# Performance work log

Measured on AMD Instinct MI355X. Metric: run time of the kernel, lower is better.

The kernel has to match this reference:

```python
import jax, jax.numpy as jnp
import numpy as np

B, S, D = 4, 4096, 1024
H, DH = 16, 64            # heads, head dim (D = H*DH)
W = 256                   # local window size; S % W == 0
HID = 2 * D               # GEGLU hidden dim
LN_EPS = 1e-5


def setup_inputs() -> dict:
    key = jax.random.key(0)
    ks = jax.random.split(key, 8)
    w = lambda k, shp: (jax.random.normal(k, shp, jnp.float32) * 0.02)
    return {
        "x": jax.random.normal(ks[0], (B, S, D), jnp.float32),
        "ln1_g": jnp.ones((D,), jnp.float32), "ln1_b": jnp.zeros((D,), jnp.float32),
        "ln2_g": jnp.ones((D,), jnp.float32), "ln2_b": jnp.zeros((D,), jnp.float32),
        "Wq": w(ks[1], (D, D)), "Wk": w(ks[2], (D, D)), "Wv": w(ks[3], (D, D)),
        "Wo": w(ks[4], (D, D)), "bo": jnp.zeros((D,), jnp.float32),
        "W1": w(ks[5], (D, 2 * HID)), "b1": jnp.zeros((2 * HID,), jnp.float32),
        "W2": w(ks[6], (HID, D)), "b2": jnp.zeros((D,), jnp.float32),
    }


def layer_norm(x, g, b):
    mu = jnp.mean(x, axis=-1, keepdims=True)
    var = jnp.mean(jnp.square(x - mu), axis=-1, keepdims=True)
    return (x - mu) * jax.lax.rsqrt(var + LN_EPS) * g + b


def local_causal_attention(x, Wq, Wk, Wv, Wo, bo):
    b, s, d = x.shape
    nw = s // W
    def split_heads(t):  # [b,s,d] -> [b,H,nw,W,DH]
        return t.reshape(b, s, H, DH).transpose(0, 2, 1, 3).reshape(b, H, nw, W, DH)
    q = split_heads(x @ Wq)
    k = split_heads(x @ Wk)
    v = split_heads(x @ Wv)
    # look_backward=1: each window attends to [prev window, current window]
    def with_prev(t):  # [b,H,nw,W,DH] -> [b,H,nw,2W,DH]
        prev = jnp.pad(t, ((0, 0), (0, 0), (1, 0), (0, 0), (0, 0)))[:, :, :-1]
        return jnp.concatenate([prev, t], axis=3)
    kc, vc = with_prev(k), with_prev(v)
    scores = jnp.einsum("bhnqd,bhnkd->bhnqk", q, kc) * (DH ** -0.5)
    # positions: qpos = n*W + i ; kpos = (n-1)*W + j, j in [0,2W)
    n = jnp.arange(nw)[:, None, None]
    i = jnp.arange(W)[None, :, None]
    j = jnp.arange(2 * W)[None, None, :]
    qpos = n * W + i
    kpos = (n - 1) * W + j
    mask = (kpos <= qpos) & (kpos >= 0)  # causal + left-edge padding
    scores = jnp.where(mask[None, None], scores, jnp.finfo(scores.dtype).min)
    attn = jax.nn.softmax(scores, axis=-1)
    out = jnp.einsum("bhnqk,bhnkd->bhnqd", attn, vc)
    out = out.reshape(b, H, s, DH).transpose(0, 2, 1, 3).reshape(b, s, d)
    return out @ Wo + bo


def geglu(x, W1, b1, W2, b2):
    h = x @ W1 + b1
    a, g = jnp.split(h, 2, axis=-1)
    return (a * jax.nn.gelu(g, approximate=False)) @ W2 + b2


def reference(x, ln1_g, ln1_b, ln2_g, ln2_b, Wq, Wk, Wv, Wo, bo, W1, b1, W2, b2):
    x = x + local_causal_attention(layer_norm(x, ln1_g, ln1_b), Wq, Wk, Wv, Wo, bo)
    x = x + geglu(layer_norm(x, ln2_g, ln2_b), W1, b1, W2, b2)
    return x
```

## Files before the change

kernel.cpp:

```cpp
#include <hip/hip_runtime.h>
#include <hip/hip_bf16.h>

typedef __attribute__((ext_vector_type(4))) float f32x4;
typedef __attribute__((ext_vector_type(8))) short bf16x8;
typedef __attribute__((ext_vector_type(8))) unsigned short u16x8;

static __device__ __forceinline__ ushort f2b(float f) {
  union { float f; unsigned u; } v; v.f = f;
  unsigned r = v.u + 0x7fffu + ((v.u >> 16) & 1u);
  return (ushort)(r >> 16);
}

static __device__ __forceinline__ float gelu_fast(float g) {
  const float c0 = 0.7978845608028654f, c1 = 0.044715f;
  const float u = c0 * (g + c1 * g * g * g);
  const float e = __expf(2.0f * u);
  const float t = 1.0f - 2.0f / (e + 1.0f);
  return 0.5f * g * (1.0f + t);
}

static __device__ __forceinline__ void gload_lds16(const void* g, void* l) {
  __builtin_amdgcn_global_load_lds(
      (__attribute__((address_space(1))) void*)(g),
      (__attribute__((address_space(3))) void*)(l), 16, 0, 0);
}

__global__ __launch_bounds__(256) void transpose_cast_kernel(
    const float* __restrict__ W, ushort* __restrict__ Wt, int K, int N) {
  __shared__ float tile[32][33];
  const int n0 = blockIdx.x * 32, k0 = blockIdx.y * 32;
  const int tx = threadIdx.x, ty = threadIdx.y;
#pragma unroll
  for (int r = 0; r < 32; r += 8)
    tile[ty + r][tx] = W[(size_t)(k0 + ty + r) * N + n0 + tx];
  __syncthreads();
#pragma unroll
  for (int r = 0; r < 32; r += 8)
    Wt[(size_t)(n0 + ty + r) * K + k0 + tx] = f2b(tile[tx][ty + r]);
}

__global__ __launch_bounds__(256) void ln_kernel(
    const float* __restrict__ x, const float* __restrict__ g,
    const float* __restrict__ bb, ushort* __restrict__ out) {
  const int row = blockIdx.x;
  const float* xr = x + (size_t)row * 1024;
  const float4 v = *(const float4*)&xr[threadIdx.x * 4];
  float s = v.x + v.y + v.z + v.w;
  float s2 = v.x * v.x + v.y * v.y + v.z * v.z + v.w * v.w;
#pragma unroll
  for (int off = 32; off > 0; off >>= 1) {
    s += __shfl_down(s, off);
    s2 += __shfl_down(s2, off);
  }
  __shared__ float red[8];
  const int lane = threadIdx.x & 63, wv = threadIdx.x >> 6;
  if (lane == 0) { red[wv] = s; red[4 + wv] = s2; }
  __syncthreads();
  s = red[0] + red[1] + red[2] + red[3];
  s2 = red[4] + red[5] + red[6] + red[7];
  const float mu = s * (1.0f / 1024.0f);
  const float rs = rsqrtf(s2 * (1.0f / 1024.0f) - mu * mu + 1e-5f);
  const int c = threadIdx.x * 4;
  ushort4 o;
  o.x = f2b((v.x - mu) * rs * g[c + 0] + bb[c + 0]);
  o.y = f2b((v.y - mu) * rs * g[c + 1] + bb[c + 1]);
  o.z = f2b((v.z - mu) * rs * g[c + 2] + bb[c + 2]);
  o.w = f2b((v.w - mu) * rs * g[c + 3] + bb[c + 3]);
  *(ushort4*)&out[(size_t)row * 1024 + c] = o;
}

template <int MODE>
__global__ __launch_bounds__(512) void gemm256_kernel(
    const ushort* __restrict__ A, const ushort* __restrict__ Bt,
    const int M, const int N, const int K,
    ushort* __restrict__ Cb, float* __restrict__ Cf,
    const float* __restrict__ bias, const float* __restrict__ res) {
  __shared__ __align__(16) ushort lds[3 * 16384];

  const int ntn = N >> 8;
  const int bn = blockIdx.x % ntn;
  const int bm = blockIdx.x / ntn;
  const int tid = threadIdx.x;
  const int l = tid & 63, w = tid >> 6;
  const int wm = w >> 2, wn = w & 3;
  const int fr = l & 15, fq = l >> 4;

  const ushort* Ab = A + (size_t)bm * 256 * K;
  const ushort* Bb = Bt + (size_t)bn * 256 * K;

  const int srow = (l >> 2);
  const int scol = (((l & 3) ^ ((l >> 3) & 3)) * 8);

  f32x4 acc[8][4];
#pragma unroll
  for (int m = 0; m < 8; m++)
#pragma unroll
    for (int n = 0; n < 4; n++) acc[m][n] = (f32x4)0.0f;

  const int NT = K >> 5;

#define STAGE256(t)                                                            \
  {                                                                            \
    const int b3 = (t) % 3;                                                    \
    const size_t kk = (size_t)(t) * 32;                                        \
    _Pragma("unroll") for (int i = 0; i < 2; i++) {                            \
      const int r = (w * 2 + i) * 16 + srow;                                   \
      gload_lds16(Ab + (size_t)r * K + kk + scol,                              \
                  &lds[b3 * 16384 + (w * 2 + i) * 512]);                       \
      gload_lds16(Bb + (size_t)r * K + kk + scol,                              \
                  &lds[b3 * 16384 + 8192 + (w * 2 + i) * 512]);                \
    }                                                                          \
  }

  STAGE256(0);
  STAGE256(1);

  for (int t = 0; t < NT; ++t) {
    if (t + 2 < NT) {
      STAGE256(t + 2);
      asm volatile("s_waitcnt vmcnt(8)" ::: "memory");
    } else if (t + 1 < NT) {
      asm volatile("s_waitcnt vmcnt(4)" ::: "memory");
    } else {
      asm volatile("s_waitcnt vmcnt(0)" ::: "memory");
    }
    __builtin_amdgcn_s_barrier();
    asm volatile("" ::: "memory");

    const ushort* La = &lds[(t % 3) * 16384];
    const ushort* Lb = La + 8192;

    bf16x8 af[8], bf[4];
#pragma unroll
    for (int m = 0; m < 8; m++) {
      const int r = wm * 128 + m * 16 + fr;
      af[m] = *(const bf16x8*)&La[r * 32 + ((fq ^ ((r >> 1) & 3)) * 8)];
    }
#pragma unroll
    for (int n = 0; n < 4; n++) {
      const int r = wn * 64 + n * 16 + fr;
      bf[n] = *(const bf16x8*)&Lb[r * 32 + ((fq ^ ((r >> 1) & 3)) * 8)];
    }

    __builtin_amdgcn_s_setprio(1);
#pragma unroll
    for (int m = 0; m < 8; m++)
#pragma unroll
      for (int n = 0; n < 4; n++)
        acc[m][n] = __builtin_amdgcn_mfma_f32_16x16x32_bf16(af[m], bf[n], acc[m][n], 0, 0, 0);
    __builtin_amdgcn_s_setprio(0);

    asm volatile("" ::: "memory");
    __builtin_amdgcn_s_barrier();
  }
#undef STAGE256

  const int rowb = bm * 256 + wm * 128 + fq * 4;
  const int colb = bn * 256 + wn * 64 + fr;
#pragma unroll
  for (int m = 0; m < 8; m++) {
#pragma unroll
    for (int n = 0; n < 4; n++) {
      const int col = colb + n * 16;
#pragma unroll
      for (int j = 0; j < 4; j++) {
        const int row = rowb + m * 16 + j;
        float vv = acc[m][n][j];
        if (MODE == 0) {
          Cb[(size_t)row * N + col] = f2b(vv);
        } else if (MODE == 2) {
          if (col < 1024) vv *= 0.125f;
          Cb[(size_t)row * N + col] = f2b(vv);
        } else {
          Cf[(size_t)row * N + col] = vv + bias[col] + res[(size_t)row * N + col];
        }
      }
    }
  }
}

__global__ __launch_bounds__(512) void gemm_geglu_kernel(
    const ushort* __restrict__ A, const ushort* __restrict__ W1t,
    const float* __restrict__ b1, ushort* __restrict__ U) {
  const int K = 1024;
  __shared__ __align__(16) ushort lds[3 * 16384];

  const int bn = blockIdx.x & 15;
  const int bm = blockIdx.x >> 4;
  const int tid = threadIdx.x;
  const int l = tid & 63, w = tid >> 6;
  const int wm = w >> 2, wn = w & 3;
  const int fr = l & 15, fq = l >> 4;

  const ushort* Ab = A + (size_t)bm * 256 * K;
  const ushort* Bab = W1t + (size_t)bn * 128 * K;
  const ushort* Bgb = W1t + (size_t)(2048 + bn * 128) * K;

  const int srow = (l >> 2);
  const int scol = (((l & 3) ^ ((l >> 3) & 3)) * 8);
  const int brow = (tid >> 2);
  const int bscol = (((tid & 3) ^ ((tid >> 3) & 3)) * 8);

  f32x4 acca[8][2], accg[8][2];
#pragma unroll
  for (int m = 0; m < 8; m++)
#pragma unroll
    for (int n = 0; n < 2; n++) { acca[m][n] = (f32x4)0.0f; accg[m][n] = (f32x4)0.0f; }

  const int NT = K >> 5;

#define STAGEGL(t)                                                             \
  {                                                                            \
    const int b3 = (t) % 3;                                                    \
    const size_t kk = (size_t)(t) * 32;                                        \
    _Pragma("unroll") for (int i = 0; i < 2; i++) {                            \
      const int r = (w * 2 + i) * 16 + srow;                                   \
      gload_lds16(Ab + (size_t)r * K + kk + scol,                              \
                  &lds[b3 * 16384 + (w * 2 + i) * 512]);                       \
    }                                                                          \
    gload_lds16(Bab + (size_t)brow * K + kk + bscol,                           \
                &lds[b3 * 16384 + 8192 + w * 512]);                            \
    gload_lds16(Bgb + (size_t)brow * K + kk + bscol,                           \
                &lds[b3 * 16384 + 12288 + w * 512]);                           \
  }

  STAGEGL(0);
  STAGEGL(1);

  for (int t = 0; t < NT; ++t) {
    if (t + 2 < NT) {
      STAGEGL(t + 2);
      asm volatile("s_waitcnt vmcnt(8)" ::: "memory");
    } else if (t + 1 < NT) {
      asm volatile("s_waitcnt vmcnt(4)" ::: "memory");
    } else {
      asm volatile("s_waitcnt vmcnt(0)" ::: "memory");
    }
    __builtin_amdgcn_s_barrier();
    asm volatile("" ::: "memory");

    const ushort* La = &lds[(t % 3) * 16384];
    const ushort* Lba = La + 8192;
    const ushort* Lbg = La + 12288;

    bf16x8 af[8], ba[2], bg[2];
#pragma unroll
    for (int m = 0; m < 8; m++) {
      const int r = wm * 128 + m * 16 + fr;
      af[m] = *(const bf16x8*)&La[r * 32 + ((fq ^ ((r >> 1) & 3)) * 8)];
    }
#pragma unroll
    for (int n = 0; n < 2; n++) {
      const int r = wn * 32 + n * 16 + fr;
      ba[n] = *(const bf16x8*)&Lba[r * 32 + ((fq ^ ((r >> 1) & 3)) * 8)];
      bg[n] = *(const bf16x8*)&Lbg[r * 32 + ((fq ^ ((r >> 1) & 3)) * 8)];
    }

    __builtin_amdgcn_s_setprio(1);
#pragma unroll
    for (int m = 0; m < 8; m++)
#pragma unroll
      for (int n = 0; n < 2; n++) {
        acca[m][n] = __builtin_amdgcn_mfma_f32_16x16x32_bf16(af[m], ba[n], acca[m][n], 0, 0, 0);
        accg[m][n] = __builtin_amdgcn_mfma_f32_16x16x32_bf16(af[m], bg[n], accg[m][n], 0, 0, 0);
      }
    __builtin_amdgcn_s_setprio(0);

    asm volatile("" ::: "memory");
    __builtin_amdgcn_s_barrier();
  }
#undef STAGEGL

  const int rowb = bm * 256 + wm * 128 + fq * 4;
  const int colb = bn * 128 + wn * 32 + fr;
#pragma unroll
  for (int m = 0; m < 8; m++) {
#pragma unroll
    for (int n = 0; n < 2; n++) {
      const int col = colb + n * 16;
      const float b1a = b1[col];
      const float b1g = b1[2048 + col];
#pragma unroll
      for (int j = 0; j < 4; j++) {
        const int row = rowb + m * 16 + j;
        const float a = acca[m][n][j] + b1a;
        const float gg = accg[m][n][j] + b1g;
        U[(size_t)row * 2048 + col] = f2b(a * gelu_fast(gg));
      }
    }
  }
}

__global__ __launch_bounds__(256, 3) void attn_kernel(
    const ushort* __restrict__ Q, const ushort* __restrict__ Kb,
    const ushort* __restrict__ Vb, ushort* __restrict__ O, const int qs) {
  const int bx = blockIdx.x;
  const int n = bx & 15;
  const int h = (bx >> 4) & 15;
  const int b = bx >> 8;
  const int tid = threadIdx.x;
  const int lane = tid & 63, wv = tid >> 6;
  const int fr = lane & 15, fq = lane >> 4;

  __shared__ __align__(16) ushort Kl[64 * 72];
  __shared__ __align__(16) ushort Vt[64 * 70];
  __shared__ __align__(16) ushort Pl[4][64 * 68];

  const size_t qrow0 = (size_t)b * 4096 + (size_t)n * 256;

  bf16x8 qf[4][2];
#pragma unroll
  for (int m = 0; m < 4; m++)
#pragma unroll
    for (int kh = 0; kh < 2; kh++)
      qf[m][kh] = *(const bf16x8*)&Q[(qrow0 + wv * 64 + m * 16 + fr) * qs + h * 64 + kh * 32 + fq * 8];

  f32x4 oacc[4][4];
#pragma unroll
  for (int m = 0; m < 4; m++)
#pragma unroll
    for (int d = 0; d < 4; d++) oacc[m][d] = (f32x4)0.0f;

  float lsum[4][4];
#pragma unroll
  for (int m = 0; m < 4; m++)
#pragma unroll
    for (int j = 0; j < 4; j++) lsum[m][j] = 0.0f;

  const int c0 = (n == 0) ? 4 : 0;
  for (int c = c0; c < 8; c++) {
    const size_t kvrow0 =
        (size_t)((long long)b * 4096 + (long long)n * 256 + (long long)c * 64 - 256);
#pragma unroll
    for (int p = 0; p < 2; p++) {
      const int s = tid + p * 256;
      const int rr = s >> 3, cs2 = s & 7;
      *(u16x8*)&Kl[rr * 72 + cs2 * 8] =
          *(const u16x8*)&Kb[(kvrow0 + rr) * qs + h * 64 + cs2 * 8];
      const u16x8 vvv = *(const u16x8*)&Vb[(kvrow0 + rr) * qs + h * 64 + cs2 * 8];
#pragma unroll
      for (int i = 0; i < 8; i++) Vt[(cs2 * 8 + i) * 70 + rr] = vvv[i];
    }
    __syncthreads();

    if (c <= wv + 4) {
      const bool diag = (c == wv + 4);
#pragma unroll
      for (int nn = 0; nn < 4; nn++) {
        f32x4 sa[4];
#pragma unroll
        for (int m = 0; m < 4; m++) sa[m] = (f32x4)0.0f;
#pragma unroll
        for (int kh = 0; kh < 2; kh++) {
          const bf16x8 bk = *(const bf16x8*)&Kl[(nn * 16 + fr) * 72 + kh * 32 + fq * 8];
#pragma unroll
          for (int m = 0; m < 4; m++)
            sa[m] = __builtin_amdgcn_mfma_f32_16x16x32_bf16(qf[m][kh], bk, sa[m], 0, 0, 0);
        }
#pragma unroll
        for (int m = 0; m < 4; m++)
#pragma unroll
          for (int j = 0; j < 4; j++) {
            float p = __expf(sa[m][j]);
            if (diag && (nn * 16 + fr > m * 16 + fq * 4 + j)) p = 0.0f;
            lsum[m][j] += p;
            Pl[wv][(m * 16 + fq * 4 + j) * 68 + nn * 16 + fr] = f2b(p);
          }
      }
      __builtin_amdgcn_s_setprio(1);
#pragma unroll
      for (int kh = 0; kh < 2; kh++) {
        bf16x8 pa[4];
#pragma unroll
        for (int m = 0; m < 4; m++)
          pa[m] = *(const bf16x8*)&Pl[wv][(m * 16 + fr) * 68 + kh * 32 + fq * 8];
#pragma unroll
        for (int d = 0; d < 4; d++) {
          const bf16x8 vb = *(const bf16x8*)&Vt[(d * 16 + fr) * 70 + kh * 32 + fq * 8];
#pragma unroll
          for (int m = 0; m < 4; m++)
            oacc[m][d] = __builtin_amdgcn_mfma_f32_16x16x32_bf16(pa[m], vb, oacc[m][d], 0, 0, 0);
        }
      }
      __builtin_amdgcn_s_setprio(0);
    }
    __syncthreads();
  }

  float rl[4][4];
#pragma unroll
  for (int m = 0; m < 4; m++)
#pragma unroll
    for (int j = 0; j < 4; j++) {
      float t = lsum[m][j];
      t += __shfl_xor(t, 1);
      t += __shfl_xor(t, 2);
      t += __shfl_xor(t, 4);
      t += __shfl_xor(t, 8);
      rl[m][j] = 1.0f / t;
    }

#pragma unroll
  for (int m = 0; m < 4; m++)
#pragma unroll
    for (int d = 0; d < 4; d++)
#pragma unroll
      for (int j = 0; j < 4; j++) {
        const float o = oacc[m][d][j] * rl[m][j];
        O[(qrow0 + wv * 64 + m * 16 + fq * 4 + j) * 1024 + h * 64 + d * 16 + fr] = f2b(o);
      }
}

extern "C" void kernel_launch(void* const* d_in, const int* in_sizes, int n_in,
                              void* d_out, int out_size, void* d_ws, size_t ws_size,
                              hipStream_t stream) {
  (void)in_sizes; (void)n_in; (void)out_size; (void)ws_size;
  const float* x     = (const float*)d_in[0];
  const float* ln1_g = (const float*)d_in[1];
  const float* ln1_b = (const float*)d_in[2];
  const float* ln2_g = (const float*)d_in[3];
  const float* ln2_b = (const float*)d_in[4];
  const float* Wq    = (const float*)d_in[5];
  const float* Wk    = (const float*)d_in[6];
  const float* Wv    = (const float*)d_in[7];
  const float* Wo    = (const float*)d_in[8];
  const float* bo    = (const float*)d_in[9];
  const float* W1    = (const float*)d_in[10];
  const float* b1    = (const float*)d_in[11];
  const float* W2    = (const float*)d_in[12];
  const float* b2    = (const float*)d_in[13];

  char* ws = (char*)d_ws;
  const size_t MB = 1ull << 20;
  ushort* WQKVT = (ushort*)(ws + 0 * MB);
  ushort* WOT = (ushort*)(ws + 6 * MB);
  ushort* W1T = (ushort*)(ws + 8 * MB);
  ushort* W2T = (ushort*)(ws + 16 * MB);
  ushort* LN1 = (ushort*)(ws + 20 * MB);
  ushort* ATT = LN1;
  ushort* QKV = (ushort*)(ws + 52 * MB);
  ushort* LN2 = (ushort*)(ws + 52 * MB);
  ushort* U   = (ushort*)(ws + 84 * MB);
  float*  X1  = (float*)d_out;
  float*  OUT = (float*)d_out;

  const dim3 tb(32, 8);
  transpose_cast_kernel<<<dim3(32, 32), tb, 0, stream>>>(Wq, WQKVT, 1024, 1024);
  transpose_cast_kernel<<<dim3(32, 32), tb, 0, stream>>>(Wk, WQKVT + (size_t)1024 * 1024, 1024, 1024);
  transpose_cast_kernel<<<dim3(32, 32), tb, 0, stream>>>(Wv, WQKVT + (size_t)2048 * 1024, 1024, 1024);
  transpose_cast_kernel<<<dim3(32, 32), tb, 0, stream>>>(Wo, WOT, 1024, 1024);
  transpose_cast_kernel<<<dim3(128, 32), tb, 0, stream>>>(W1, W1T, 1024, 4096);
  transpose_cast_kernel<<<dim3(32, 64), tb, 0, stream>>>(W2, W2T, 2048, 1024);

  ln_kernel<<<16384, 256, 0, stream>>>(x, ln1_g, ln1_b, LN1);

  gemm256_kernel<2><<<64 * 12, 512, 0, stream>>>(LN1, WQKVT, 16384, 3072, 1024,
                                                 QKV, nullptr, nullptr, nullptr);

  attn_kernel<<<1024, 256, 0, stream>>>(QKV, QKV + 1024, QKV + 2048, ATT, 3072);

  gemm256_kernel<1><<<64 * 4, 512, 0, stream>>>(ATT, WOT, 16384, 1024, 1024,
                                                nullptr, X1, bo, x);

  ln_kernel<<<16384, 256, 0, stream>>>(X1, ln2_g, ln2_b, LN2);

  gemm_geglu_kernel<<<64 * 16, 512, 0, stream>>>(LN2, W1T, b1, U);

  gemm256_kernel<1><<<64 * 4, 512, 0, stream>>>(U, W2T, 16384, 1024, 2048,
                                                nullptr, OUT, b2, X1);
}
```

Measured before the change: 557.0 us.

## Restructure GEMM main loops into 4-stage split-phase pipeline with XCD swizzle

Result: no change. 550.9 us (-1.1%).

```diff
diff --git a/kernel.cpp b/kernel.cpp
--- a/kernel.cpp
+++ b/kernel.cpp
@@ -23,6 +23,13 @@
   __builtin_amdgcn_global_load_lds(
       (__attribute__((address_space(1))) void*)(g),
       (__attribute__((address_space(3))) void*)(l), 16, 0, 0);
+}
+
+#define MFMA_BF16 __builtin_amdgcn_mfma_f32_16x16x32_bf16
+
+static __device__ __forceinline__ int xcd_swz(int bid, int nwg) {
+  const int q = nwg >> 3;
+  return (bid & 7) * q + (bid >> 3);
 }
 
 __global__ __launch_bounds__(256) void transpose_cast_kernel(
@@ -70,26 +77,40 @@
 }
 
 template <int MODE>
-__global__ __launch_bounds__(512) void gemm256_kernel(
+__global__ __launch_bounds__(512, 2) void gemm256_kernel(
     const ushort* __restrict__ A, const ushort* __restrict__ Bt,
     const int M, const int N, const int K,
     ushort* __restrict__ Cb, float* __restrict__ Cf,
     const float* __restrict__ bias, const float* __restrict__ res) {
-  __shared__ __align__(16) ushort lds[3 * 16384];
-
+  __shared__ __align__(16) ushort lds[65536];
+
+  const int nwg = gridDim.x;
+  const int bid = xcd_swz((int)blockIdx.x, nwg);
   const int ntn = N >> 8;
-  const int bn = blockIdx.x % ntn;
-  const int bm = blockIdx.x / ntn;
+  const int bn = bid % ntn;
+  const int bm = bid / ntn;
   const int tid = threadIdx.x;
   const int l = tid & 63, w = tid >> 6;
   const int wm = w >> 2, wn = w & 3;
   const int fr = l & 15, fq = l >> 4;
 
-  const ushort* Ab = A + (size_t)bm * 256 * K;
-  const ushort* Bb = Bt + (size_t)bn * 256 * K;
-
-  const int srow = (l >> 2);
-  const int scol = (((l & 3) ^ ((l >> 3) & 3)) * 8);
+  const char* ldsc = (const char*)lds;
+  char* ldscw = (char*)lds;
+
+  const unsigned sl16 = (unsigned)((fq ^ ((fr >> 2) & 3)) * 16);
+  const unsigned aOff = (unsigned)(wm * 8192 + fr * 64) + sl16;
+  const unsigned bOff = 16384u + (unsigned)(wn * 4096 + fr * 64) + sl16;
+  const unsigned aB0 = 0 * 32768u + aOff, aB1 = 1 * 32768u + aOff;
+  const unsigned aB2 = 2 * 32768u + aOff, aB3 = 3 * 32768u + aOff;
+  const unsigned bB0 = 0 * 32768u + bOff, bB1 = 1 * 32768u + bOff;
+  const unsigned bB2 = 2 * 32768u + bOff, bB3 = 3 * 32768u + bOff;
+
+  const int srow = tid >> 2;
+  const int scol = (((tid & 3) ^ ((tid >> 4) & 3)) * 8);
+  const ushort* qA0 = A + (size_t)bm * 256 * K + (size_t)srow * K + scol;
+  const ushort* qA1 = qA0 + (size_t)128 * K;
+  const ushort* qB0 = Bt + (size_t)bn * 256 * K + (size_t)srow * K + scol;
+  const ushort* qB1 = qB0 + (size_t)128 * K;
 
   f32x4 acc[8][4];
 #pragma unroll
@@ -98,62 +119,74 @@
     for (int n = 0; n < 4; n++) acc[m][n] = (f32x4)0.0f;
 
   const int NT = K >> 5;
-
-#define STAGE256(t)                                                            \
+  const unsigned wlds = (unsigned)(w * 1024);
+
+#define GB(aBv, bBv, WSB, DOSTG, VMM, KOFF)                                    \
   {                                                                            \
-    const int b3 = (t) % 3;                                                    \
-    const size_t kk = (size_t)(t) * 32;                                        \
-    _Pragma("unroll") for (int i = 0; i < 2; i++) {                            \
-      const int r = (w * 2 + i) * 16 + srow;                                   \
-      gload_lds16(Ab + (size_t)r * K + kk + scol,                              \
-                  &lds[b3 * 16384 + (w * 2 + i) * 512]);                       \
-      gload_lds16(Bb + (size_t)r * K + kk + scol,                              \
-                  &lds[b3 * 16384 + 8192 + (w * 2 + i) * 512]);                \
-    }                                                                          \
-  }
-
-  STAGE256(0);
-  STAGE256(1);
-
-  for (int t = 0; t < NT; ++t) {
-    if (t + 2 < NT) {
-      STAGE256(t + 2);
-      asm volatile("s_waitcnt vmcnt(8)" ::: "memory");
-    } else if (t + 1 < NT) {
-      asm volatile("s_waitcnt vmcnt(4)" ::: "memory");
-    } else {
-      asm volatile("s_waitcnt vmcnt(0)" ::: "memory");
-    }
-    __builtin_amdgcn_s_barrier();
-    asm volatile("" ::: "memory");
-
-    const ushort* La = &lds[(t % 3) * 16384];
-    const ushort* Lb = La + 8192;
-
-    bf16x8 af[8], bf[4];
-#pragma unroll
-    for (int m = 0; m < 8; m++) {
-      const int r = wm * 128 + m * 16 + fr;
-      af[m] = *(const bf16x8*)&La[r * 32 + ((fq ^ ((r >> 1) & 3)) * 8)];
-    }
-#pragma unroll
-    for (int n = 0; n < 4; n++) {
-      const int r = wn * 64 + n * 16 + fr;
-      bf[n] = *(const bf16x8*)&Lb[r * 32 + ((fq ^ ((r >> 1) & 3)) * 8)];
-    }
-
-    __builtin_amdgcn_s_setprio(1);
-#pragma unroll
-    for (int m = 0; m < 8; m++)
-#pragma unroll
-      for (int n = 0; n < 4; n++)
-        acc[m][n] = __builtin_amdgcn_mfma_f32_16x16x32_bf16(af[m], bf[n], acc[m][n], 0, 0, 0);
-    __builtin_amdgcn_s_setprio(0);
-
-    asm volatile("" ::: "memory");
-    __builtin_amdgcn_s_barrier();
-  }
-#undef STAGE256
+    bf16x8 af[8], bfv[4];                                                      \
+    if (DOSTG) {                                                               \
+      gload_lds16(qA0 + (KOFF), ldscw + (WSB) + wlds);                         \
+      gload_lds16(qA1 + (KOFF), ldscw + (WSB) + 8192 + wlds);                  \
+    }                                                                          \
+    _Pragma("unroll") for (int m = 0; m < 8; m++)                              \
+      af[m] = *(const bf16x8*)(ldsc + (aBv) + m * 1024);                       \
+    bfv[0] = *(const bf16x8*)(ldsc + (bBv));                                   \
+    bfv[1] = *(const bf16x8*)(ldsc + (bBv) + 1024);                            \
+    __builtin_amdgcn_s_barrier();                                              \
+    asm volatile("" ::: "memory");                                             \
+    __builtin_amdgcn_s_setprio(1);                                             \
+    _Pragma("unroll") for (int m = 0; m < 8; m++) {                            \
+      acc[m][0] = MFMA_BF16(af[m], bfv[0], acc[m][0], 0, 0, 0);                \
+      acc[m][1] = MFMA_BF16(af[m], bfv[1], acc[m][1], 0, 0, 0);                \
+    }                                                                          \
+    __builtin_amdgcn_s_setprio(0);                                             \
+    asm volatile("" ::: "memory");                                             \
+    __builtin_amdgcn_s_barrier();                                              \
+    if (DOSTG) {                                                               \
+      gload_lds16(qB0 + (KOFF), ldscw + (WSB) + 16384 + wlds);                 \
+      gload_lds16(qB1 + (KOFF), ldscw + (WSB) + 24576 + wlds);                 \
+    }                                                                          \
+    bfv[2] = *(const bf16x8*)(ldsc + (bBv) + 2048);                            \
+    bfv[3] = *(const bf16x8*)(ldsc + (bBv) + 3072);                            \
+    if ((VMM) == 0) { asm volatile("s_waitcnt vmcnt(4)" ::: "memory"); }       \
+    else if ((VMM) == 1) { asm volatile("s_waitcnt vmcnt(0)" ::: "memory"); }  \
+    __builtin_amdgcn_s_barrier();                                              \
+    asm volatile("" ::: "memory");                                             \
+    __builtin_amdgcn_s_setprio(1);                                             \
+    _Pragma("unroll") for (int m = 0; m < 8; m++) {                            \
+      acc[m][2] = MFMA_BF16(af[m], bfv[2], acc[m][2], 0, 0, 0);                \
+      acc[m][3] = MFMA_BF16(af[m], bfv[3], acc[m][3], 0, 0, 0);                \
+    }                                                                          \
+    __builtin_amdgcn_s_setprio(0);                                             \
+    asm volatile("" ::: "memory");                                             \
+    __builtin_amdgcn_s_barrier();                                              \
+  }
+
+  gload_lds16(qA0, ldscw + 0 + wlds);
+  gload_lds16(qA1, ldscw + 8192 + wlds);
+  gload_lds16(qB0, ldscw + 16384 + wlds);
+  gload_lds16(qB1, ldscw + 24576 + wlds);
+  gload_lds16(qA0 + 32, ldscw + 32768 + wlds);
+  gload_lds16(qA1 + 32, ldscw + 32768 + 8192 + wlds);
+  gload_lds16(qB0 + 32, ldscw + 32768 + 16384 + wlds);
+  gload_lds16(qB1 + 32, ldscw + 32768 + 24576 + wlds);
+  qA0 += 64; qA1 += 64; qB0 += 64; qB1 += 64;
+  asm volatile("s_waitcnt vmcnt(4)" ::: "memory");
+  __builtin_amdgcn_s_barrier();
+  asm volatile("" ::: "memory");
+
+  for (int t = 0; t + 8 <= NT; t += 4) {
+    GB(aB0, bB0, 2 * 32768u, true, 0, 0);
+    GB(aB1, bB1, 3 * 32768u, true, 0, 32);
+    GB(aB2, bB2, 0 * 32768u, true, 0, 64);
+    GB(aB3, bB3, 1 * 32768u, true, 0, 96);
+    qA0 += 128; qA1 += 128; qB0 += 128; qB1 += 128;
+  }
+  GB(aB0, bB0, 2 * 32768u, true, 0, 0);
+  GB(aB1, bB1, 3 * 32768u, true, 0, 32);
+  GB(aB2, bB2, 0u, false, 1, 0);
+  GB(aB3, bB3, 0u, false, 2, 0);
+#undef GB
 
   const int rowb = bm * 256 + wm * 128 + fq * 4;
   const int colb = bn * 256 + wn * 64 + fr;
@@ -179,27 +212,38 @@
   }
 }
 
-__global__ __launch_bounds__(512) void gemm_geglu_kernel(
+__global__ __launch_bounds__(512, 2) void gemm_geglu_kernel(
     const ushort* __restrict__ A, const ushort* __restrict__ W1t,
     const float* __restrict__ b1, ushort* __restrict__ U) {
   const int K = 1024;
-  __shared__ __align__(16) ushort lds[3 * 16384];
-
-  const int bn = blockIdx.x & 15;
-  const int bm = blockIdx.x >> 4;
+  __shared__ __align__(16) ushort lds[65536];
+
+  const int nwg = gridDim.x;
+  const int bid = xcd_swz((int)blockIdx.x, nwg);
+  const int bn = bid & 15;
+  const int bm = bid >> 4;
   const int tid = threadIdx.x;
   const int l = tid & 63, w = tid >> 6;
   const int wm = w >> 2, wn = w & 3;
   const int fr = l & 15, fq = l >> 4;
 
-  const ushort* Ab = A + (size_t)bm * 256 * K;
-  const ushort* Bab = W1t + (size_t)bn * 128 * K;
-  const ushort* Bgb = W1t + (size_t)(2048 + bn * 128) * K;
-
-  const int srow = (l >> 2);
-  const int scol = (((l & 3) ^ ((l >> 3) & 3)) * 8);
-  const int brow = (tid >> 2);
-  const int bscol = (((tid & 3) ^ ((tid >> 3) & 3)) * 8);
+  const char* ldsc = (const char*)lds;
+  char* ldscw = (char*)lds;
+
+  const unsigned sl16 = (unsigned)((fq ^ ((fr >> 2) & 3)) * 16);
+  const unsigned aOff = (unsigned)(wm * 8192 + fr * 64) + sl16;
+  const unsigned baOff = 16384u + (unsigned)(wn * 2048 + fr * 64) + sl16;
+  const unsigned aB0 = 0 * 32768u + aOff, aB1 = 1 * 32768u + aOff;
+  const unsigned aB2 = 2 * 32768u + aOff, aB3 = 3 * 32768u + aOff;
+  const unsigned cB0 = 0 * 32768u + baOff, cB1 = 1 * 32768u + baOff;
+  const unsigned cB2 = 2 * 32768u + baOff, cB3 = 3 * 32768u + baOff;
+
+  const int srow = tid >> 2;
+  const int scol = (((tid & 3) ^ ((tid >> 4) & 3)) * 8);
+  const ushort* qA0 = A + (size_t)bm * 256 * K + (size_t)srow * K + scol;
+  const ushort* qA1 = qA0 + (size_t)128 * K;
+  const ushort* qBa = W1t + (size_t)bn * 128 * K + (size_t)srow * K + scol;
+  const ushort* qBg = qBa + (size_t)2048 * K;
 
   f32x4 acca[8][2], accg[8][2];
 #pragma unroll
@@ -208,68 +252,74 @@
     for (int n = 0; n < 2; n++) { acca[m][n] = (f32x4)0.0f; accg[m][n] = (f32x4)0.0f; }
 
   const int NT = K >> 5;
-
-#define STAGEGL(t)                                                             \
+  const unsigned wlds = (unsigned)(w * 1024);
+
+#define GLB(aBv, cBv, WSB, DOSTG, VMM, KOFF)                                   \
   {                                                                            \
-    const int b3 = (t) % 3;                                                    \
-    const size_t kk = (size_t)(t) * 32;                                        \
-    _Pragma("unroll") for (int i = 0; i < 2; i++) {                            \
-      const int r = (w * 2 + i) * 16 + srow;                                   \
-      gload_lds16(Ab + (size_t)r * K + kk + scol,                              \
-                  &lds[b3 * 16384 + (w * 2 + i) * 512]);                       \
-    }                                                                          \
-    gload_lds16(Bab + (size_t)brow * K + kk + bscol,                           \
-                &lds[b3 * 16384 + 8192 + w * 512]);                            \
-    gload_lds16(Bgb + (size_t)brow * K + kk + bscol,                           \
-                &lds[b3 * 16384 + 12288 + w * 512]);                           \
-  }
-
-  STAGEGL(0);
-  STAGEGL(1);
-
-  for (int t = 0; t < NT; ++t) {
-    if (t + 2 < NT) {
-      STAGEGL(t + 2);
-      asm volatile("s_waitcnt vmcnt(8)" ::: "memory");
-    } else if (t + 1 < NT) {
-      asm volatile("s_waitcnt vmcnt(4)" ::: "memory");
-    } else {
-      asm volatile("s_waitcnt vmcnt(0)" ::: "memory");
-    }
-    __builtin_amdgcn_s_barrier();
-    asm volatile("" ::: "memory");
-
-    const ushort* La = &lds[(t % 3) * 16384];
-    const ushort* Lba = La + 8192;
-    const ushort* Lbg = La + 12288;
-
-    bf16x8 af[8], ba[2], bg[2];
-#pragma unroll
-    for (int m = 0; m < 8; m++) {
-      const int r = wm * 128 + m * 16 + fr;
-      af[m] = *(const bf16x8*)&La[r * 32 + ((fq ^ ((r >> 1) & 3)) * 8)];
-    }
-#pragma unroll
-    for (int n = 0; n < 2; n++) {
-      const int r = wn * 32 + n * 16 + fr;
-      ba[n] = *(const bf16x8*)&Lba[r * 32 + ((fq ^ ((r >> 1) & 3)) * 8)];
-      bg[n] = *(const bf16x8*)&Lbg[r * 32 + ((fq ^ ((r >> 1) & 3)) * 8)];
-    }
-
-    __builtin_amdgcn_s_setprio(1);
-#pragma unroll
-    for (int m = 0; m < 8; m++)
-#pragma unroll
-      for (int n = 0; n < 2; n++) {
-        acca[m][n] = __builtin_amdgcn_mfma_f32_16x16x32_bf16(af[m], ba[n], acca[m][n], 0, 0, 0);
-        accg[m][n] = __builtin_amdgcn_mfma_f32_16x16x32_bf16(af[m], bg[n], accg[m][n], 0, 0, 0);
-      }
-    __builtin_amdgcn_s_setprio(0);
-
-    asm volatile("" ::: "memory");
-    __builtin_amdgcn_s_barrier();
-  }
-#undef STAGEGL
+    bf16x8 af[8], ba[2], bg[2];                                                \
+    if (DOSTG) {                                                               \
+      gload_lds16(qA0 + (KOFF), ldscw + (WSB) + wlds);                         \
+      gload_lds16(qA1 + (KOFF), ldscw + (WSB) + 8192 + wlds);                  \
+    }                                                                          \
+    _Pragma("unroll") for (int m = 0; m < 8; m++)                              \
+      af[m] = *(const bf16x8*)(ldsc + (aBv) + m * 1024);                       \
+    ba[0] = *(const bf16x8*)(ldsc + (cBv));                                    \
+    ba[1] = *(const bf16x8*)(ldsc + (cBv) + 1024);                             \
+    __builtin_amdgcn_s_barrier();                                              \
+    asm volatile("" ::: "memory");                                             \
+    __builtin_amdgcn_s_setprio(1);                                             \
+    _Pragma("unroll") for (int m = 0; m < 8; m++) {                            \
+      acca[m][0] = MFMA_BF16(af[m], ba[0], acca[m][0], 0, 0, 0);               \
+      acca[m][1] = MFMA_BF16(af[m], ba[1], acca[m][1], 0, 0, 0);               \
+    }                                                                          \
+    __builtin_amdgcn_s_setprio(0);                                             \
+    asm volatile("" ::: "memory");                                             \
+    __builtin_amdgcn_s_barrier();                                              \
+    if (DOSTG) {                                                               \
+      gload_lds16(qBa + (KOFF), ldscw + (WSB) + 16384 + wlds);                 \
+      gload_lds16(qBg + (KOFF), ldscw + (WSB) + 24576 + wlds);                 \
+    }                                                                          \
+    bg[0] = *(const bf16x8*)(ldsc + (cBv) + 8192);                             \
+    bg[1] = *(const bf16x8*)(ldsc + (cBv) + 8192 + 1024);                      \
+    if ((VMM) == 0) { asm volatile("s_waitcnt vmcnt(4)" ::: "memory"); }       \
+    else if ((VMM) == 1) { asm volatile("s_waitcnt vmcnt(0)" ::: "memory"); }  \
+    __builtin_amdgcn_s_barrier();                                              \
+    asm volatile("" ::: "memory");                                             \
+    __builtin_amdgcn_s_setprio(1);                                             \
+    _Pragma("unroll") for (int m = 0; m < 8; m++) {                            \
+      accg[m][0] = MFMA_BF16(af[m], bg[0], accg[m][0], 0, 0, 0);               \
+      accg[m][1] = MFMA_BF16(af[m], bg[1], accg[m][1], 0, 0, 0);               \
+    }                                                                          \
+    __builtin_amdgcn_s_setprio(0);                                             \
+    asm volatile("" ::: "memory");                                             \
+    __builtin_amdgcn_s_barrier();                                              \
+  }
+
+  gload_lds16(qA0, ldscw + 0 + wlds);
+  gload_lds16(qA1, ldscw + 8192 + wlds);
+  gload_lds16(qBa, ldscw + 16384 + wlds);
+  gload_lds16(qBg, ldscw + 24576 + wlds);
+  gload_lds16(qA0 + 32, ldscw + 32768 + wlds);
+  gload_lds16(qA1 + 32, ldscw + 32768 + 8192 + wlds);
+  gload_lds16(qBa + 32, ldscw + 32768 + 16384 + wlds);
+  gload_lds16(qBg + 32, ldscw + 32768 + 24576 + wlds);
+  qA0 += 64; qA1 += 64; qBa += 64; qBg += 64;
+  asm volatile("s_waitcnt vmcnt(4)" ::: "memory");
+  __builtin_amdgcn_s_barrier();
+  asm volatile("" ::: "memory");
+
+  for (int t = 0; t + 8 <= NT; t += 4) {
+    GLB(aB0, cB0, 2 * 32768u, true, 0, 0);
+    GLB(aB1, cB1, 3 * 32768u, true, 0, 32);
+    GLB(aB2, cB2, 0 * 32768u, true, 0, 64);
+    GLB(aB3, cB3, 1 * 32768u, true, 0, 96);
+    qA0 += 128; qA1 += 128; qBa += 128; qBg += 128;
+  }
+  GLB(aB0, cB0, 2 * 32768u, true, 0, 0);
+  GLB(aB1, cB1, 3 * 32768u, true, 0, 32);
+  GLB(aB2, cB2, 0u, false, 1, 0);
+  GLB(aB3, cB3, 0u, false, 2, 0);
+#undef GLB
 
   const int rowb = bm * 256 + wm * 128 + fq * 4;
   const int colb = bn * 128 + wn * 32 + fr;
@@ -355,7 +405,7 @@
           const bf16x8 bk = *(const bf16x8*)&Kl[(nn * 16 + fr) * 72 + kh * 32 + fq * 8];
 #pragma unroll
           for (int m = 0; m < 4; m++)
-            sa[m] = __builtin_amdgcn_mfma_f32_16x16x32_bf16(qf[m][kh], bk, sa[m], 0, 0, 0);
+            sa[m] = MFMA_BF16(qf[m][kh], bk, sa[m], 0, 0, 0);
         }
 #pragma unroll
         for (int m = 0; m < 4; m++)
@@ -379,7 +429,7 @@
           const bf16x8 vb = *(const bf16x8*)&Vt[(d * 16 + fr) * 70 + kh * 32 + fq * 8];
 #pragma unroll
           for (int m = 0; m < 4; m++)
-            oacc[m][d] = __builtin_amdgcn_mfma_f32_16x16x32_bf16(pa[m], vb, oacc[m][d], 0, 0, 0);
+            oacc[m][d] = MFMA_BF16(pa[m], vb, oacc[m][d], 0, 0, 0);
         }
       }
       __builtin_amdgcn_s_setprio(0);
```
